# Kernel optimization log

Hardware: AMD Instinct MI355X
Metric: run time of the kernel (lower is better)

## Reference

```python
import jax, jax.numpy as jnp
import numpy as np


def setup_inputs() -> dict:
    key = jax.random.key(0)
    ks = jax.random.split(key, 6)
    B, L, D, H, W = 32, 1024, 128, 128, 9
    F = D + W  # feature dim after one-hot positional embed
    rn = lambda k, shape, s: (jax.random.normal(k, shape, jnp.float32) * s)
    return {
        "embeddings": rn(ks[0], (B, L, D), 1.0),
        "masks": jnp.ones((B, L), jnp.float32),  # unused in math (as in source)
        "w1_w": rn(ks[1], (F, H), 0.05),
        "w1_b": jnp.zeros((H,), jnp.float32),
        "w2_w": rn(ks[2], (F, H), 0.05),
        "w2_b": jnp.zeros((H,), jnp.float32),
        "v_w": rn(ks[3], (H, 1), 0.05),
        "v_b": jnp.zeros((1,), jnp.float32),
        "cnn_w": rn(ks[4], (F * W, H), 0.02),
        "cnn_b": jnp.zeros((H,), jnp.float32),
        "window_size": 9,
    }


def reference(embeddings, masks, w1_w, w1_b, w2_w, w2_b, v_w, v_b, cnn_w, cnn_b, window_size):
    # Vectorized form of the per-position loop in LocalConvolutionLayer.forward.
    B, L, D = embeddings.shape
    W = window_size
    half = W // 2
    # Zero-pad then gather all sliding windows at once: [B, L, W, D]
    padded = jnp.pad(embeddings, ((0, 0), (half, half), (0, 0)))
    idx = jnp.arange(L)[:, None] + jnp.arange(W)[None, :]  # [L, W]
    win = padded[:, idx, :]
    # One-hot within-window positional embedding, concatenated on channels -> F = D + W
    pos = jnp.broadcast_to(jnp.eye(W, dtype=embeddings.dtype), (B, L, W, W))
    ctx = jnp.concatenate([win, pos], axis=-1)  # [B, L, W, F]
    ent = ctx[:, :, half, :]                    # center token, [B, L, F]
    # AttentionLayer: v(tanh(w1(ent)[:,None] + w2(ctx)))
    re = ent @ w1_w + w1_b                      # [B, L, H]
    rc = ctx @ w2_w + w2_b                      # [B, L, W, H]
    scores = jnp.tanh(re[:, :, None, :] + rc) @ v_w + v_b  # [B, L, W, 1]
    weights = jax.nn.softmax(scores, axis=2)
    out = (weights * ctx).reshape(B, L, W * ctx.shape[-1])  # [B, L, W*F]
    return out @ cnn_w + cnn_b                  # [B, L, H]
```

## Files before the change

kernel.cpp:

```cpp
#include <hip/hip_runtime.h>
#include <hip/hip_bf16.h>


typedef __attribute__((ext_vector_type(8))) short bf16x8;
typedef __attribute__((ext_vector_type(4))) float f32x4;

#define LL 1024

__device__ __forceinline__ unsigned short f2bf(float f) {
  unsigned int u = __float_as_uint(f);
  u = u + 0x7FFFu + ((u >> 16) & 1u);
  return (unsigned short)(u >> 16);
}
__device__ __forceinline__ float bf2f(unsigned short us) {
  return __uint_as_float(((unsigned int)us) << 16);
}
__device__ __forceinline__ float fast_tanh(float x) {
  float e = __expf(2.f * x);
  return 1.f - 2.f * __builtin_amdgcn_rcpf(e + 1.f);
}

__global__ __launch_bounds__(256) void prep_kernel(
    const float* __restrict__ w1, const float* __restrict__ w2,
    const float* __restrict__ cnn,
    unsigned short* __restrict__ W12Bt, unsigned short* __restrict__ CwBt) {
  int gid = blockIdx.x * 256 + threadIdx.x;
  if (blockIdx.x < 128) {
    int n = gid >> 7, d = gid & 127;
    float v = (n < 128) ? w1[d * 128 + n] : w2[d * 128 + (n - 128)];
    W12Bt[n * 128 + d] = f2bf(v);
  } else {
    int idx = gid - 32768;
    int h = idx / 1152;
    int c = idx - h * 1152;
    int w = c >> 7, d = c & 127;
    CwBt[h * 1152 + c] = f2bf(cnn[(w * 137 + d) * 128 + h]);
  }
}

__global__ __launch_bounds__(512, 2) void mega_kernel(
    const float* __restrict__ emb,
    const unsigned short* __restrict__ W12Bt,
    const unsigned short* __restrict__ CwBt,
    const float* __restrict__ w1, const float* __restrict__ w1b,
    const float* __restrict__ w2, const float* __restrict__ w2b,
    const float* __restrict__ vw,
    const float* __restrict__ cnn, const float* __restrict__ cnnb,
    float* __restrict__ out) {
  extern __shared__ __align__(16) unsigned char smem[];
  uint4* E   = (uint4*)smem;
  float* wtT = (float*)(smem + 36864);
  uint4* HB  = (uint4*)(smem + 41472);
  unsigned short* H = (unsigned short*)(smem + 41472);

  int tid = threadIdx.x;
  int bid = blockIdx.x;
  int b = bid >> 3, l0 = (bid & 7) << 7;
  int lane = tid & 63, wid = tid >> 6;
  int l15 = lane & 15, l4 = lane >> 4;

  #pragma unroll
  for (int s = 0; s < 5; ++s) {
    int i = tid + s * 512;
    if (i < 2304) {
      int er = i >> 4, g = i & 15;
      int t = l0 + er - 4;
      uint4 v = {0u, 0u, 0u, 0u};
      if (t >= 0 && t < LL) {
        const float4* src = (const float4*)(emb + ((size_t)(b * LL + t) << 7) + g * 8);
        float4 x0 = src[0], x1 = src[1];
        v.x = f2bf(x0.x) | ((unsigned)f2bf(x0.y) << 16);
        v.y = f2bf(x0.z) | ((unsigned)f2bf(x0.w) << 16);
        v.z = f2bf(x1.x) | ((unsigned)f2bf(x1.y) << 16);
        v.w = f2bf(x1.z) | ((unsigned)f2bf(x1.w) << 16);
      }
      E[er * 16 + (g ^ (er & 7))] = v;
    }
  }
  #pragma unroll
  for (int s = 0; s < 8; ++s) {
    int i = tid + s * 512;
    int n = i >> 4, g = i & 15;
    HB[n * 16 + (g ^ (n & 7))] = *(const uint4*)(W12Bt + n * 128 + g * 8);
  }
  __syncthreads();

  const bf16x8* Eb = (const bf16x8*)E;
  const bf16x8* Wb = (const bf16x8*)HB;
  f32x4 acc[3][8];
  #pragma unroll
  for (int it = 0; it < 3; ++it) {
    int rt = wid + it * 8;
    if (rt < 18) {
      int part = rt >= 9;
      int er0 = (part ? rt - 9 : rt) * 16;
      int nbase = part << 7;
      #pragma unroll
      for (int nn = 0; nn < 8; ++nn) acc[it][nn] = (f32x4){0.f, 0.f, 0.f, 0.f};
      #pragma unroll
      for (int kk = 0; kk < 4; ++kk) {
        int er = er0 + l15;
        bf16x8 aF = Eb[er * 16 + ((kk * 4 + l4) ^ (er & 7))];
        #pragma unroll
        for (int nn = 0; nn < 8; ++nn) {
          int n = nbase + nn * 16 + l15;
          bf16x8 bF = Wb[n * 16 + ((kk * 4 + l4) ^ (n & 7))];
          acc[it][nn] = __builtin_amdgcn_mfma_f32_16x16x32_bf16(aF, bF, acc[it][nn], 0, 0, 0);
        }
      }
    }
  }
  __syncthreads();
  #pragma unroll
  for (int it = 0; it < 3; ++it) {
    int rt = wid + it * 8;
    if (rt < 18) {
      int part = rt >= 9;
      int er0 = (part ? rt - 9 : rt) * 16;
      #pragma unroll
      for (int nn = 0; nn < 8; ++nn)
        #pragma unroll
        for (int j = 0; j < 4; ++j)
          H[part * 18432 + (er0 + l4 * 4 + j) * 128 + nn * 16 + l15] = f2bf(acc[it][nn][j]);
    }
  }
  __syncthreads();

  {
    float c1_0 = w1[132 * 128 + lane] + w1b[lane];
    float c1_1 = w1[132 * 128 + 64 + lane] + w1b[64 + lane];
    float vw0 = vw[lane], vw1 = vw[64 + lane];
    float pw0[9], pw1[9];
    #pragma unroll
    for (int w = 0; w < 9; ++w) {
      pw0[w] = w2[(128 + w) * 128 + lane] + w2b[lane];
      pw1[w] = w2[(128 + w) * 128 + 64 + lane] + w2b[64 + lane];
    }
    const unsigned short* H1 = H;
    const unsigned short* H2 = H + 18432;
    for (int rr = 0; rr < 16; ++rr) {
      int r = wid * 16 + rr;
      float f0 = bf2f(H1[(r + 4) * 128 + lane]) + c1_0;
      float f1 = bf2f(H1[(r + 4) * 128 + 64 + lane]) + c1_1;
      float s[9];
      #pragma unroll
      for (int w = 0; w < 9; ++w) {
        float g0 = bf2f(H2[(r + w) * 128 + lane]);
        float g1 = bf2f(H2[(r + w) * 128 + 64 + lane]);
        float v = fast_tanh(f0 + g0 + pw0[w]) * vw0 + fast_tanh(f1 + g1 + pw1[w]) * vw1;
        #pragma unroll
        for (int off = 32; off; off >>= 1) v += __shfl_xor(v, off, 64);
        s[w] = v;
      }
      float mx = s[0];
      #pragma unroll
      for (int w = 1; w < 9; ++w) mx = fmaxf(mx, s[w]);
      float sum = 0.f;
      #pragma unroll
      for (int w = 0; w < 9; ++w) { s[w] = __expf(s[w] - mx); sum += s[w]; }
      float inv = __builtin_amdgcn_rcpf(sum);
      float wv = s[0];
      #pragma unroll
      for (int w = 1; w < 9; ++w) wv = (lane == w) ? s[w] : wv;
      if (lane < 9) wtT[lane * 128 + r] = wv * inv;
    }
  }

  int wr = wid >> 2, wc = wid & 3;
  int h0 = wc * 32 + l15;
  float cb0 = cnnb[h0], cb1 = cnnb[h0 + 16];
  f32x4 fin[4][2];
  #pragma unroll
  for (int m = 0; m < 4; ++m)
    #pragma unroll
    for (int n = 0; n < 2; ++n) fin[m][n] = (f32x4){0.f, 0.f, 0.f, 0.f};
  const bf16x8* Bb = (const bf16x8*)HB;

  for (int w = 0; w < 9; ++w) {
    __syncthreads();
    #pragma unroll
    for (int s = 0; s < 4; ++s) {
      int i = tid + s * 512;
      int hh = i >> 4, g = i & 15;
      HB[hh * 16 + (g ^ (hh & 7))] = *(const uint4*)(CwBt + hh * 1152 + w * 128 + g * 8);
    }
    float cp0 = cnn[(w * 138 + 128) * 128 + h0];
    float cp1 = cnn[(w * 138 + 128) * 128 + h0 + 16];
    __syncthreads();
    f32x4 tmp[4][2];
    #pragma unroll
    for (int m = 0; m < 4; ++m)
      #pragma unroll
      for (int n = 0; n < 2; ++n) tmp[m][n] = (f32x4){0.f, 0.f, 0.f, 0.f};
    #pragma unroll
    for (int kk = 0; kk < 4; ++kk) {
      bf16x8 aF[4];
      #pragma unroll
      for (int m = 0; m < 4; ++m) {
        int er = wr * 64 + m * 16 + l15 + w;
        aF[m] = Eb[er * 16 + ((kk * 4 + l4) ^ (er & 7))];
      }
      #pragma unroll
      for (int n = 0; n < 2; ++n) {
        int hh = wc * 32 + n * 16 + l15;
        bf16x8 bF = Bb[hh * 16 + ((kk * 4 + l4) ^ (hh & 7))];
        #pragma unroll
        for (int m = 0; m < 4; ++m)
          tmp[m][n] = __builtin_amdgcn_mfma_f32_16x16x32_bf16(aF[m], bF, tmp[m][n], 0, 0, 0);
      }
    }
    #pragma unroll
    for (int m = 0; m < 4; ++m) {
      f32x4 wt4 = *(const f32x4*)(wtT + w * 128 + wr * 64 + m * 16 + l4 * 4);
      #pragma unroll
      for (int j = 0; j < 4; ++j) {
        fin[m][0][j] += wt4[j] * (tmp[m][0][j] + cp0);
        fin[m][1][j] += wt4[j] * (tmp[m][1][j] + cp1);
      }
    }
  }
  #pragma unroll
  for (int m = 0; m < 4; ++m)
    #pragma unroll
    for (int j = 0; j < 4; ++j) {
      int r = wr * 64 + m * 16 + l4 * 4 + j;
      size_t o = ((size_t)(b * LL + l0 + r) << 7) + h0;
      out[o]      = fin[m][0][j] + cb0;
      out[o + 16] = fin[m][1][j] + cb1;
    }
}

extern "C" void kernel_launch(void* const* d_in, const int* in_sizes, int n_in,
                              void* d_out, int out_size, void* d_ws, size_t ws_size,
                              hipStream_t stream) {
  const float* emb  = (const float*)d_in[0];
  const float* w1   = (const float*)d_in[2];
  const float* w1b  = (const float*)d_in[3];
  const float* w2   = (const float*)d_in[4];
  const float* w2b  = (const float*)d_in[5];
  const float* vw   = (const float*)d_in[6];
  const float* cnn  = (const float*)d_in[8];
  const float* cnnb = (const float*)d_in[9];
  float* out = (float*)d_out;

  char* ws = (char*)d_ws;
  unsigned short* W12Bt = (unsigned short*)(ws);
  unsigned short* CwBt  = (unsigned short*)(ws + 65536);

  prep_kernel<<<704, 256, 0, stream>>>(w1, w2, cnn, W12Bt, CwBt);
  mega_kernel<<<256, 512, 115200, stream>>>(emb, W12Bt, CwBt, w1, w1b, w2, w2b,
                                            vw, cnn, cnnb, out);
}
```

Baseline: 137.4 us.

## Halve row tile to 64, stream weights from global, restructure attention scoring

Each block now handles 64 sequence rows instead of 128, giving 512 blocks with smaller LDS (about 69KB), and launch bounds are raised to allow more resident blocks per CU. The W1/W2 and CNN weight tiles are no longer staged into LDS; MFMA B-fragments are read straight from global/L2, which removes the per-window LDS fills and their barriers. The attention scoring is rewritten: tanh constants are folded into exp2 scaling, positional biases are precomputed into LDS, and each row is split across 16 lanes with a 4-step shuffle reduction instead of a full-wavefront reduction. In exchange, the 8-row halo is recomputed in twice as many blocks, and the global B-operand loads may add latency.

```diff
diff --git a/kernel.cpp b/kernel.cpp
--- a/kernel.cpp
+++ b/kernel.cpp
@@ -6,6 +6,7 @@
 typedef __attribute__((ext_vector_type(4))) float f32x4;
 
 #define LL 1024
+#define TANHK 2.885390081777927f
 
 __device__ __forceinline__ unsigned short f2bf(float f) {
   unsigned int u = __float_as_uint(f);
@@ -14,10 +15,6 @@
 }
 __device__ __forceinline__ float bf2f(unsigned short us) {
   return __uint_as_float(((unsigned int)us) << 16);
-}
-__device__ __forceinline__ float fast_tanh(float x) {
-  float e = __expf(2.f * x);
-  return 1.f - 2.f * __builtin_amdgcn_rcpf(e + 1.f);
 }
 
 __global__ __launch_bounds__(256) void prep_kernel(
@@ -38,7 +35,7 @@
   }
 }
 
-__global__ __launch_bounds__(512, 2) void mega_kernel(
+__global__ __launch_bounds__(512, 4) void mega_kernel(
     const float* __restrict__ emb,
     const unsigned short* __restrict__ W12Bt,
     const unsigned short* __restrict__ CwBt,
@@ -48,25 +45,26 @@
     const float* __restrict__ cnn, const float* __restrict__ cnnb,
     float* __restrict__ out) {
   extern __shared__ __align__(16) unsigned char smem[];
-  uint4* E   = (uint4*)smem;
-  float* wtT = (float*)(smem + 36864);
-  uint4* HB  = (uint4*)(smem + 41472);
-  unsigned short* H = (unsigned short*)(smem + 41472);
+  uint4* E            = (uint4*)smem;
+  unsigned short* Hs  = (unsigned short*)(smem + 20480);
+  float* pwL          = (float*)(smem + 61440);
+  float* vwL          = (float*)(smem + 66048);
+  float* wtT          = (float*)(smem + 66560);
 
   int tid = threadIdx.x;
   int bid = blockIdx.x;
-  int b = bid >> 3, l0 = (bid & 7) << 7;
+  int b = bid >> 4, l0 = (bid & 15) << 6;
   int lane = tid & 63, wid = tid >> 6;
   int l15 = lane & 15, l4 = lane >> 4;
 
   #pragma unroll
   for (int s = 0; s < 5; ++s) {
     int i = tid + s * 512;
-    if (i < 2304) {
+    if (i < 1280) {
       int er = i >> 4, g = i & 15;
       int t = l0 + er - 4;
       uint4 v = {0u, 0u, 0u, 0u};
-      if (t >= 0 && t < LL) {
+      if (er < 72 && t >= 0 && t < LL) {
         const float4* src = (const float4*)(emb + ((size_t)(b * LL + t) << 7) + g * 8);
         float4 x0 = src[0], x1 = src[1];
         v.x = f2bf(x0.x) | ((unsigned)f2bf(x0.y) << 16);
@@ -75,143 +73,146 @@
         v.w = f2bf(x1.z) | ((unsigned)f2bf(x1.w) << 16);
       }
       E[er * 16 + (g ^ (er & 7))] = v;
-    }
-  }
-  #pragma unroll
-  for (int s = 0; s < 8; ++s) {
-    int i = tid + s * 512;
-    int n = i >> 4, g = i & 15;
-    HB[n * 16 + (g ^ (n & 7))] = *(const uint4*)(W12Bt + n * 128 + g * 8);
+    } else if (i < 2432) {
+      int idx = i - 1280;
+      int w = idx >> 7, h = idx & 127;
+      pwL[idx] = TANHK * (w2[(128 + w) * 128 + h] + w2b[h] +
+                          w1[132 * 128 + h] + w1b[h]);
+    } else {
+      int h = i - 2432;
+      vwL[h] = vw[h];
+    }
   }
   __syncthreads();
 
   const bf16x8* Eb = (const bf16x8*)E;
-  const bf16x8* Wb = (const bf16x8*)HB;
-  f32x4 acc[3][8];
-  #pragma unroll
-  for (int it = 0; it < 3; ++it) {
-    int rt = wid + it * 8;
-    if (rt < 18) {
-      int part = rt >= 9;
-      int er0 = (part ? rt - 9 : rt) * 16;
-      int nbase = part << 7;
-      #pragma unroll
-      for (int nn = 0; nn < 8; ++nn) acc[it][nn] = (f32x4){0.f, 0.f, 0.f, 0.f};
+  #pragma unroll
+  for (int jj = 0; jj < 2; ++jj) {
+    int job = wid + jj * 8;
+    if (job < 10) {
+      int part = job >= 5;
+      int er0 = (job - part * 5) * 16;
+      f32x4 acc[8];
+      #pragma unroll
+      for (int nn = 0; nn < 8; ++nn) acc[nn] = (f32x4){0.f, 0.f, 0.f, 0.f};
       #pragma unroll
       for (int kk = 0; kk < 4; ++kk) {
+        int gk = kk * 4 + l4;
         int er = er0 + l15;
-        bf16x8 aF = Eb[er * 16 + ((kk * 4 + l4) ^ (er & 7))];
+        bf16x8 aF = Eb[er * 16 + (gk ^ (er & 7))];
         #pragma unroll
         for (int nn = 0; nn < 8; ++nn) {
-          int n = nbase + nn * 16 + l15;
-          bf16x8 bF = Wb[n * 16 + ((kk * 4 + l4) ^ (n & 7))];
-          acc[it][nn] = __builtin_amdgcn_mfma_f32_16x16x32_bf16(aF, bF, acc[it][nn], 0, 0, 0);
-        }
-      }
+          bf16x8 bF = *(const bf16x8*)(W12Bt +
+              (size_t)((part << 7) + nn * 16 + l15) * 128 + gk * 8);
+          acc[nn] = __builtin_amdgcn_mfma_f32_16x16x32_bf16(aF, bF, acc[nn], 0, 0, 0);
+        }
+      }
+      unsigned short* Hp = Hs + part * 10240;
+      #pragma unroll
+      for (int nn = 0; nn < 8; ++nn)
+        #pragma unroll
+        for (int j = 0; j < 4; ++j) {
+          int i2 = er0 + l4 * 4 + j;
+          Hp[i2 * 128 + ((nn * 16 + l15) ^ (l4 << 4))] = f2bf(TANHK * acc[nn][j]);
+        }
     }
   }
   __syncthreads();
-  #pragma unroll
-  for (int it = 0; it < 3; ++it) {
-    int rt = wid + it * 8;
-    if (rt < 18) {
-      int part = rt >= 9;
-      int er0 = (part ? rt - 9 : rt) * 16;
-      #pragma unroll
-      for (int nn = 0; nn < 8; ++nn)
-        #pragma unroll
-        for (int j = 0; j < 4; ++j)
-          H[part * 18432 + (er0 + l4 * 4 + j) * 128 + nn * 16 + l15] = f2bf(acc[it][nn][j]);
+
+  {
+    int q = lane >> 4, u = lane & 15, u8 = u * 8;
+    const unsigned short* Hs1 = Hs;
+    const unsigned short* Hs2 = Hs + 10240;
+    #pragma unroll
+    for (int pass = 0; pass < 2; ++pass) {
+      int r = wid * 8 + pass * 4 + q;
+      int fi = r + 4;
+      int fxor = ((fi >> 2) & 3) << 4;
+      bf16x8 fraw = *(const bf16x8*)&Hs1[fi * 128 + (u8 ^ fxor)];
+      float fr[8];
+      #pragma unroll
+      for (int j = 0; j < 8; ++j) fr[j] = bf2f((unsigned short)fraw[j]);
+      f32x4 vr0 = *(const f32x4*)&vwL[u8];
+      f32x4 vr1 = *(const f32x4*)&vwL[u8 + 4];
+      float sc[9];
+      #pragma unroll
+      for (int w = 0; w < 9; ++w) {
+        int gi = r + w;
+        int gxor = ((gi >> 2) & 3) << 4;
+        bf16x8 graw = *(const bf16x8*)&Hs2[gi * 128 + (u8 ^ gxor)];
+        f32x4 pw0 = *(const f32x4*)&pwL[w * 128 + u8];
+        f32x4 pw1 = *(const f32x4*)&pwL[w * 128 + u8 + 4];
+        float a = 0.f;
+        #pragma unroll
+        for (int j = 0; j < 4; ++j) {
+          float e = exp2f(fr[j] + bf2f((unsigned short)graw[j]) + pw0[j]);
+          a = fmaf(vr0[j], __builtin_amdgcn_rcpf(1.f + e), a);
+        }
+        #pragma unroll
+        for (int j = 0; j < 4; ++j) {
+          float e = exp2f(fr[4 + j] + bf2f((unsigned short)graw[4 + j]) + pw1[j]);
+          a = fmaf(vr1[j], __builtin_amdgcn_rcpf(1.f + e), a);
+        }
+        a += __shfl_xor(a, 1, 64);
+        a += __shfl_xor(a, 2, 64);
+        a += __shfl_xor(a, 4, 64);
+        a += __shfl_xor(a, 8, 64);
+        sc[w] = a;
+      }
+      float mn = sc[0];
+      #pragma unroll
+      for (int w = 1; w < 9; ++w) mn = fminf(mn, sc[w]);
+      float p[9], sum = 0.f;
+      #pragma unroll
+      for (int w = 0; w < 9; ++w) { p[w] = exp2f(TANHK * (mn - sc[w])); sum += p[w]; }
+      float inv = __builtin_amdgcn_rcpf(sum);
+      if (u < 9) {
+        float wv = p[0];
+        #pragma unroll
+        for (int w = 1; w < 9; ++w) wv = (u == w) ? p[w] : wv;
+        wtT[u * 68 + r] = wv * inv;
+      }
     }
   }
   __syncthreads();
-
-  {
-    float c1_0 = w1[132 * 128 + lane] + w1b[lane];
-    float c1_1 = w1[132 * 128 + 64 + lane] + w1b[64 + lane];
-    float vw0 = vw[lane], vw1 = vw[64 + lane];
-    float pw0[9], pw1[9];
-    #pragma unroll
-    for (int w = 0; w < 9; ++w) {
-      pw0[w] = w2[(128 + w) * 128 + lane] + w2b[lane];
-      pw1[w] = w2[(128 + w) * 128 + 64 + lane] + w2b[64 + lane];
-    }
-    const unsigned short* H1 = H;
-    const unsigned short* H2 = H + 18432;
-    for (int rr = 0; rr < 16; ++rr) {
-      int r = wid * 16 + rr;
-      float f0 = bf2f(H1[(r + 4) * 128 + lane]) + c1_0;
-      float f1 = bf2f(H1[(r + 4) * 128 + 64 + lane]) + c1_1;
-      float s[9];
-      #pragma unroll
-      for (int w = 0; w < 9; ++w) {
-        float g0 = bf2f(H2[(r + w) * 128 + lane]);
-        float g1 = bf2f(H2[(r + w) * 128 + 64 + lane]);
-        float v = fast_tanh(f0 + g0 + pw0[w]) * vw0 + fast_tanh(f1 + g1 + pw1[w]) * vw1;
-        #pragma unroll
-        for (int off = 32; off; off >>= 1) v += __shfl_xor(v, off, 64);
-        s[w] = v;
-      }
-      float mx = s[0];
-      #pragma unroll
-      for (int w = 1; w < 9; ++w) mx = fmaxf(mx, s[w]);
-      float sum = 0.f;
-      #pragma unroll
-      for (int w = 0; w < 9; ++w) { s[w] = __expf(s[w] - mx); sum += s[w]; }
-      float inv = __builtin_amdgcn_rcpf(sum);
-      float wv = s[0];
-      #pragma unroll
-      for (int w = 1; w < 9; ++w) wv = (lane == w) ? s[w] : wv;
-      if (lane < 9) wtT[lane * 128 + r] = wv * inv;
-    }
-  }
 
   int wr = wid >> 2, wc = wid & 3;
   int h0 = wc * 32 + l15;
-  float cb0 = cnnb[h0], cb1 = cnnb[h0 + 16];
-  f32x4 fin[4][2];
-  #pragma unroll
-  for (int m = 0; m < 4; ++m)
+  f32x4 fin[2][2];
+  #pragma unroll
+  for (int m = 0; m < 2; ++m)
     #pragma unroll
     for (int n = 0; n < 2; ++n) fin[m][n] = (f32x4){0.f, 0.f, 0.f, 0.f};
-  const bf16x8* Bb = (const bf16x8*)HB;
-
+  #pragma unroll
   for (int w = 0; w < 9; ++w) {
-    __syncthreads();
-    #pragma unroll
-    for (int s = 0; s < 4; ++s) {
-      int i = tid + s * 512;
-      int hh = i >> 4, g = i & 15;
-      HB[hh * 16 + (g ^ (hh & 7))] = *(const uint4*)(CwBt + hh * 1152 + w * 128 + g * 8);
+    f32x4 tmp[2][2];
+    #pragma unroll
+    for (int m = 0; m < 2; ++m)
+      #pragma unroll
+      for (int n = 0; n < 2; ++n) tmp[m][n] = (f32x4){0.f, 0.f, 0.f, 0.f};
+    #pragma unroll
+    for (int kk = 0; kk < 4; ++kk) {
+      int gk = kk * 4 + l4;
+      bf16x8 aF[2];
+      #pragma unroll
+      for (int m = 0; m < 2; ++m) {
+        int er = wr * 32 + m * 16 + l15 + w;
+        aF[m] = Eb[er * 16 + (gk ^ (er & 7))];
+      }
+      #pragma unroll
+      for (int n = 0; n < 2; ++n) {
+        int hh = wc * 32 + n * 16 + l15;
+        bf16x8 bF = *(const bf16x8*)(CwBt + (size_t)hh * 1152 + w * 128 + gk * 8);
+        #pragma unroll
+        for (int m = 0; m < 2; ++m)
+          tmp[m][n] = __builtin_amdgcn_mfma_f32_16x16x32_bf16(aF[m], bF, tmp[m][n], 0, 0, 0);
+      }
     }
     float cp0 = cnn[(w * 138 + 128) * 128 + h0];
     float cp1 = cnn[(w * 138 + 128) * 128 + h0 + 16];
-    __syncthreads();
-    f32x4 tmp[4][2];
-    #pragma unroll
-    for (int m = 0; m < 4; ++m)
-      #pragma unroll
-      for (int n = 0; n < 2; ++n) tmp[m][n] = (f32x4){0.f, 0.f, 0.f, 0.f};
-    #pragma unroll
-    for (int kk = 0; kk < 4; ++kk) {
-      bf16x8 aF[4];
-      #pragma unroll
-      for (int m = 0; m < 4; ++m) {
-        int er = wr * 64 + m * 16 + l15 + w;
-        aF[m] = Eb[er * 16 + ((kk * 4 + l4) ^ (er & 7))];
-      }
-      #pragma unroll
-      for (int n = 0; n < 2; ++n) {
-        int hh = wc * 32 + n * 16 + l15;
-        bf16x8 bF = Bb[hh * 16 + ((kk * 4 + l4) ^ (hh & 7))];
-        #pragma unroll
-        for (int m = 0; m < 4; ++m)
-          tmp[m][n] = __builtin_amdgcn_mfma_f32_16x16x32_bf16(aF[m], bF, tmp[m][n], 0, 0, 0);
-      }
-    }
-    #pragma unroll
-    for (int m = 0; m < 4; ++m) {
-      f32x4 wt4 = *(const f32x4*)(wtT + w * 128 + wr * 64 + m * 16 + l4 * 4);
+    #pragma unroll
+    for (int m = 0; m < 2; ++m) {
+      f32x4 wt4 = *(const f32x4*)&wtT[w * 68 + wr * 32 + m * 16 + l4 * 4];
       #pragma unroll
       for (int j = 0; j < 4; ++j) {
         fin[m][0][j] += wt4[j] * (tmp[m][0][j] + cp0);
@@ -219,11 +220,12 @@
       }
     }
   }
-  #pragma unroll
-  for (int m = 0; m < 4; ++m)
+  float cb0 = cnnb[h0], cb1 = cnnb[h0 + 16];
+  #pragma unroll
+  for (int m = 0; m < 2; ++m)
     #pragma unroll
     for (int j = 0; j < 4; ++j) {
-      int r = wr * 64 + m * 16 + l4 * 4 + j;
+      int r = wr * 32 + m * 16 + l4 * 4 + j;
       size_t o = ((size_t)(b * LL + l0 + r) << 7) + h0;
       out[o]      = fin[m][0][j] + cb0;
       out[o + 16] = fin[m][1][j] + cb1;
@@ -248,6 +250,6 @@
   unsigned short* CwBt  = (unsigned short*)(ws + 65536);
 
   prep_kernel<<<704, 256, 0, stream>>>(w1, w2, cnn, W12Bt, CwBt);
-  mega_kernel<<<256, 512, 115200, stream>>>(emb, W12Bt, CwBt, w1, w1b, w2, w2b,
-                                            vw, cnn, cnnb, out);
-}
+  mega_kernel<<<512, 512, 69008, stream>>>(emb, W12Bt, CwBt, w1, w1b, w2, w2b,
+                                           vw, cnn, cnnb, out);
+}
```

Result: slower. 153.7 us (+11.8%).
